# Kernel optimization log

Measured on AMD Instinct MI355X. Metric: run time of the kernel, lower is better.

Reference implementation:

```python
import jax, jax.numpy as jnp
import numpy as np
import math

NUM_HEADS = 16
NUM_KV_HEADS = 4
HEAD_DIM = 128
ROPE_THETA = 10000.0


def _rope(x, cos, sin):
    # x: [b, h, s, d]; cos/sin: [1, 1, s, d//2]
    half = x.shape[-1] // 2
    x1, x2 = x[..., :half], x[..., half:]
    return jnp.concatenate([x1 * cos - x2 * sin, x2 * cos + x1 * sin], axis=-1)


def setup_inputs() -> dict:
    key = jax.random.key(0)
    ks = jax.random.split(key, 5)
    B, S, H = 2, 2048, 2048
    scale_qk = (2.0 / (H + H)) ** 0.5
    scale_kv = (2.0 / (H + NUM_KV_HEADS * HEAD_DIM)) ** 0.5
    return {
        "hidden_states": jax.random.normal(ks[0], (B, S, H), jnp.float32),
        "Wq": jax.random.normal(ks[1], (NUM_HEADS * HEAD_DIM, H), jnp.float32) * scale_qk,
        "Wk": jax.random.normal(ks[2], (NUM_KV_HEADS * HEAD_DIM, H), jnp.float32) * scale_kv,
        "Wv": jax.random.normal(ks[3], (NUM_KV_HEADS * HEAD_DIM, H), jnp.float32) * scale_kv,
        "Wo": jax.random.normal(ks[4], (NUM_HEADS * HEAD_DIM, H), jnp.float32) * scale_qk,
    }


def reference(hidden_states, Wq, Wk, Wv, Wo):
    B, S, H = hidden_states.shape
    hd = HEAD_DIM

    q = (hidden_states @ Wq.T).reshape(B, S, NUM_HEADS, hd).transpose(0, 2, 1, 3)
    k = (hidden_states @ Wk.T).reshape(B, S, NUM_KV_HEADS, hd).transpose(0, 2, 1, 3)
    v = (hidden_states @ Wv.T).reshape(B, S, NUM_KV_HEADS, hd).transpose(0, 2, 1, 3)

    # RoPE (half-split variant, as in module)
    inv_freq = 1.0 / (ROPE_THETA ** (jnp.arange(0, hd, 2, dtype=jnp.float32) / hd))
    pos = jnp.arange(S, dtype=jnp.float32)
    freqs = pos[:, None] * inv_freq[None, :]           # [S, hd//2]
    cos = jnp.cos(freqs)[None, None]                   # [1,1,S,hd//2]
    sin = jnp.sin(freqs)[None, None]
    q = _rope(q, cos, sin)
    k = _rope(k, cos, sin)

    # GQA: repeat kv heads (repeat_interleave semantics)
    n_rep = NUM_HEADS // NUM_KV_HEADS
    k = jnp.repeat(k, n_rep, axis=1)
    v = jnp.repeat(v, n_rep, axis=1)

    scores = jnp.einsum("bhqd,bhkd->bhqk", q, k) / math.sqrt(hd)
    attn = jax.nn.softmax(scores, axis=-1)
    out = jnp.einsum("bhqk,bhkd->bhqd", attn, v)
    out = out.transpose(0, 2, 1, 3).reshape(B, S, NUM_HEADS * hd)
    return out @ Wo.T
```

## Files before the change

kernel.cpp:

```cpp
#include <hip/hip_runtime.h>
#include <cstdint>
#include <cstddef>

typedef __bf16 bf16x8 __attribute__((ext_vector_type(8)));
typedef __bf16 bf16x4 __attribute__((ext_vector_type(4)));
typedef float  f32x4  __attribute__((ext_vector_type(4)));

__device__ __forceinline__ void gload_lds16(const void* g, void* l) {
    __builtin_amdgcn_global_load_lds(
        (const __attribute__((address_space(1))) void*)g,
        (__attribute__((address_space(3))) void*)l, 16, 0, 0);
}

#define VM6B asm volatile("s_waitcnt vmcnt(6) lgkmcnt(0)\ns_barrier" ::: "memory")
#define VM4B asm volatile("s_waitcnt vmcnt(4) lgkmcnt(0)\ns_barrier" ::: "memory")
#define VM0B asm volatile("s_waitcnt vmcnt(0) lgkmcnt(0)\ns_barrier" ::: "memory")
#define BARO asm volatile("s_barrier" ::: "memory")
#define WAITB4 asm volatile("s_waitcnt vmcnt(4) lgkmcnt(0)\ns_barrier" ::: "memory")
#define WAITB0 asm volatile("s_waitcnt vmcnt(0) lgkmcnt(0)\ns_barrier" ::: "memory")

#define SEQ 2048
#define NH 16
#define NKV 4
#define HD 128

__global__ __launch_bounds__(256) void cvt_all(const float* __restrict__ hs,
                                               const float* __restrict__ wq,
                                               const float* __restrict__ wk,
                                               const float* __restrict__ wv,
                                               const float* __restrict__ wo,
                                               __bf16* __restrict__ hB,
                                               __bf16* __restrict__ WqkB,
                                               __bf16* __restrict__ WvB,
                                               __bf16* __restrict__ WoB) {
    int bid = blockIdx.x;
    const float* in; __bf16* out; int base;
    if (bid < 8192)        { in = hs; out = hB;                   base = bid; }
    else if (bid < 12288)  { in = wq; out = WqkB;                 base = bid - 8192; }
    else if (bid < 13312)  { in = wk; out = WqkB + 2048 * 2048;   base = bid - 12288; }
    else if (bid < 14336)  { in = wv; out = WvB;                  base = bid - 13312; }
    else                   { in = wo; out = WoB;                  base = bid - 14336; }
    int i = base * 256 + threadIdx.x;
    float4 v = ((const float4*)in)[i];
    bf16x4 o = { (__bf16)v.x, (__bf16)v.y, (__bf16)v.z, (__bf16)v.w };
    ((bf16x4*)out)[i] = o;
}

__device__ __forceinline__ void stage_half(const __bf16* __restrict__ M,
                                           char* dbuf, int bmn, int k0, int half,
                                           int wave, int lane) {
    char* hb = dbuf + (half & 1) * 32768 + (half >> 1) * 16384;
    int kbase = k0 + (half >> 1) * 32;
#pragma unroll
    for (int g = 0; g < 2; ++g) {
        int c = wave * 2 + g;
        int row = (c & 3) * 64 + lane;
        int ks = c >> 2;
        gload_lds16(M + (size_t)(bmn + row) * 2048 + kbase + ks * 8, hb + c * 1024);
    }
}

template <int KS, int MH>
__device__ __forceinline__ void phase_mfma(const __bf16* bA, const __bf16* bB,
                                           int quad, int l16, int wr128, int colbase,
                                           bf16x8 (&bq)[4], f32x4 acc[8][4]) {
    bf16x8 af[4];
#pragma unroll
    for (int ii = 0; ii < 4; ++ii)
        af[ii] = *(const bf16x8*)(bA + (KS * 4 + quad) * 2048 +
                                  (wr128 + (MH * 4 + ii) * 16 + l16) * 8);
    if (MH == 0) {
#pragma unroll
        for (int j = 0; j < 4; ++j)
            bq[j] = *(const bf16x8*)(bB + (KS * 4 + quad) * 2048 +
                                     (colbase + (j & 1) * 16 + (j >> 1) * 64 + l16) * 8);
    }
    __builtin_amdgcn_s_setprio(1);
#pragma unroll
    for (int ii = 0; ii < 4; ++ii)
#pragma unroll
        for (int j = 0; j < 4; ++j)
            acc[MH * 4 + ii][j] = __builtin_amdgcn_mfma_f32_16x16x32_bf16(
                af[ii], bq[j], acc[MH * 4 + ii][j], 0, 0, 0);
    __builtin_amdgcn_s_setprio(0);
}

__device__ __forceinline__ void gemm_core(const __bf16* __restrict__ A,
                                          const __bf16* __restrict__ B,
                                          char* lds, int bm, int bn,
                                          int wave, int lane, int quad, int l16,
                                          int wr128, int colbase, f32x4 acc[8][4]) {
    const int NT = 32;
    stage_half(A, lds, bm, 0, 0, wave, lane);
    stage_half(B, lds, bn, 0, 1, wave, lane);
    stage_half(A, lds, bm, 0, 2, wave, lane);
    stage_half(B, lds, bn, 0, 3, wave, lane);
    int cur = 0;
    for (int t = 0; t < NT - 1; ++t) {
        const __bf16* bA = (const __bf16*)(lds + cur * 65536);
        const __bf16* bB = (const __bf16*)(lds + cur * 65536 + 32768);
        char* nb = lds + (cur ^ 1) * 65536;
        int k1 = (t + 1) * 64;
        bf16x8 bq[4];
        stage_half(A, nb, bm, k1, 0, wave, lane);
        VM6B;
        phase_mfma<0, 0>(bA, bB, quad, l16, wr128, colbase, bq, acc);
        stage_half(B, nb, bn, k1, 1, wave, lane);
        BARO;
        phase_mfma<0, 1>(bA, bB, quad, l16, wr128, colbase, bq, acc);
        stage_half(A, nb, bm, k1, 2, wave, lane);
        VM6B;
        phase_mfma<1, 0>(bA, bB, quad, l16, wr128, colbase, bq, acc);
        stage_half(B, nb, bn, k1, 3, wave, lane);
        BARO;
        phase_mfma<1, 1>(bA, bB, quad, l16, wr128, colbase, bq, acc);
        cur ^= 1;
    }
    {
        const __bf16* bA = (const __bf16*)(lds + cur * 65536);
        const __bf16* bB = (const __bf16*)(lds + cur * 65536 + 32768);
        bf16x8 bq[4];
        VM4B;
        phase_mfma<0, 0>(bA, bB, quad, l16, wr128, colbase, bq, acc);
        phase_mfma<0, 1>(bA, bB, quad, l16, wr128, colbase, bq, acc);
        VM0B;
        phase_mfma<1, 0>(bA, bB, quad, l16, wr128, colbase, bq, acc);
        phase_mfma<1, 1>(bA, bB, quad, l16, wr128, colbase, bq, acc);
    }
}

__global__ __launch_bounds__(512, 2) void qkv_gemm(const __bf16* __restrict__ hB,
                                                   const __bf16* __restrict__ Wqk,
                                                   const __bf16* __restrict__ Wv,
                                                   __bf16* __restrict__ Qr,
                                                   __bf16* __restrict__ Kr,
                                                   __bf16* __restrict__ VT) {
    __shared__ __align__(16) char lds[2 * 65536];
    const int tid = threadIdx.x;
    const int wave = tid >> 6, lane = tid & 63;
    const int quad = lane >> 4, l16 = lane & 15;
    const int wr = wave >> 2, wc = wave & 3;
    int wg = blockIdx.y * 16 + blockIdx.x;
    wg = (wg & 7) * 24 + (wg >> 3);
    const int x = wg & 15, y = wg >> 4;
    const bool isVT = (y >= 10);
    const bool isQ = (y < 8);

    const __bf16* Amat = isVT ? Wv : hB;
    const __bf16* Bmat = isVT ? hB : (isQ ? Wqk : Wqk + 2048 * 2048);
    const int bm = isVT ? (y - 10) * 256 : x * 256;
    const int bn = isVT ? x * 256 : (isQ ? y * 256 : (y - 8) * 256);

    const int wr128 = wr * 128;
    const int colbase = (wc >> 1) * 128 + (wc & 1) * 32;

    f32x4 acc[8][4] = {};
    gemm_core(Amat, Bmat, lds, bm, bn, wave, lane, quad, l16, wr128, colbase, acc);

    if (isVT) {
#pragma unroll
        for (int i = 0; i < 8; ++i)
#pragma unroll
            for (int j = 0; j < 4; ++j) {
                int row = bm + wr128 + i * 16 + quad * 4;
                int col = bn + colbase + (j & 1) * 16 + (j >> 1) * 64 + l16;
#pragma unroll
                for (int r = 0; r < 4; ++r)
                    VT[(size_t)(row + r) * 4096 + col] = (__bf16)acc[i][j][r];
            }
    } else {
        __bf16* outp = isQ ? Qr : Kr;
        const float sc = isQ ? 0.1275255128608411f : 1.0f;
        const int nh = isQ ? NH : NKV;
        const int hh = (isQ ? y * 2 : (y - 8) * 2) + (wc >> 1);
#pragma unroll
        for (int j2 = 0; j2 < 2; ++j2) {
            int d = (wc & 1) * 32 + j2 * 16 + l16;
            float inv = exp2f(-(float)d * 0.2076205059304601f);
#pragma unroll
            for (int i = 0; i < 8; ++i)
#pragma unroll
                for (int r = 0; r < 4; ++r) {
                    int m = bm + wr128 + i * 16 + quad * 4 + r;
                    int s = m & (SEQ - 1), b = m >> 11;
                    float f = (float)s * inv;
                    float c = __cosf(f) * sc, sn = __sinf(f) * sc;
                    float x1 = acc[i][j2][r], x2 = acc[i][j2 + 2][r];
                    size_t rb = ((size_t)(b * nh + hh) * SEQ + s) * HD;
                    outp[rb + d]      = (__bf16)(x1 * c - x2 * sn);
                    outp[rb + d + 64] = (__bf16)(x2 * c + x1 * sn);
                }
        }
    }
}

__global__ __launch_bounds__(512, 1) void gemm_bt_f32(const __bf16* __restrict__ A,
                                                      const __bf16* __restrict__ W,
                                                      float* __restrict__ C) {
    __shared__ __align__(16) char lds[3 * 49152];
    const int tid = threadIdx.x;
    const int wave = tid >> 6, lane = tid & 63;
    const int quad = lane >> 4, l16 = lane & 15;
    const int wr = wave >> 2, wc = wave & 3;
    int wg = blockIdx.y * 32 + blockIdx.x;
    wg = (wg & 7) * 32 + (wg >> 3);
    const int bm = (wg & 31) * 128, bn = (wg >> 5) * 256;

    f32x4 acc[4][4] = {};

    auto stageT = [&](int sb, int k0) {
        char* dst = lds + sb * 49152;
#pragma unroll
        for (int tt = 0; tt < 6; ++tt) {
            int c = wave * 6 + tt;
            if (c < 16) {
                int row = ((c & 1) << 6) + lane;
                gload_lds16(A + (size_t)(bm + row) * 2048 + k0 + (c >> 1) * 8,
                            dst + c * 1024);
            } else {
                int vc = c - 16;
                int row = ((vc & 3) << 6) + lane;
                gload_lds16(W + (size_t)(bn + row) * 2048 + k0 + (vc >> 2) * 8,
                            dst + 16384 + vc * 1024);
            }
        }
    };

    auto computeT = [&](int cb2) {
        const __bf16* bA = (const __bf16*)(lds + cb2 * 49152);
        const __bf16* bB = bA + 8192;
#pragma unroll
        for (int ks = 0; ks < 2; ++ks) {
            bf16x8 af[4], bq[4];
#pragma unroll
            for (int i = 0; i < 4; ++i)
                af[i] = *(const bf16x8*)(bA + (ks * 4 + quad) * 1024 +
                                         (wr * 64 + i * 16 + l16) * 8);
#pragma unroll
            for (int j = 0; j < 4; ++j)
                bq[j] = *(const bf16x8*)(bB + (ks * 4 + quad) * 2048 +
                                         (wc * 64 + j * 16 + l16) * 8);
            __builtin_amdgcn_s_setprio(1);
#pragma unroll
            for (int i = 0; i < 4; ++i)
#pragma unroll
                for (int j = 0; j < 4; ++j)
                    acc[i][j] = __builtin_amdgcn_mfma_f32_16x16x32_bf16(
                        af[i], bq[j], acc[i][j], 0, 0, 0);
            __builtin_amdgcn_s_setprio(0);
        }
    };

    stageT(0, 0);
    stageT(1, 64);
    int cb = 0;
    for (int t = 0; t < 31; ++t) {
        VM6B;
        if (t < 30) {
            int sb = cb + 2; if (sb >= 3) sb -= 3;
            stageT(sb, (t + 2) * 64);
        }
        computeT(cb);
        if (++cb == 3) cb = 0;
    }
    VM0B;
    computeT(cb);

#pragma unroll
    for (int i = 0; i < 4; ++i)
#pragma unroll
        for (int j = 0; j < 4; ++j) {
            int row = bm + wr * 64 + i * 16 + quad * 4;
            int col = bn + wc * 64 + j * 16 + l16;
#pragma unroll
            for (int r = 0; r < 4; ++r)
                C[(size_t)(row + r) * 2048 + col] = acc[i][j][r];
        }
}

__global__ __launch_bounds__(256, 2) void attn_kernel(const __bf16* __restrict__ Q,
                                                      const __bf16* __restrict__ Kr,
                                                      const __bf16* __restrict__ VT,
                                                      __bf16* __restrict__ AO) {
    __shared__ __align__(16) char ring[3 * 16384];
    __shared__ __align__(16) __bf16 Pb[4][32][40];

    const int tid = threadIdx.x;
    const int wave = tid >> 6, lane = tid & 63;
    const int quad = lane >> 4, l16 = lane & 15;
    int wg = (blockIdx.z * 16 + blockIdx.y) * 16 + blockIdx.x;
    wg = (wg & 7) * 64 + (wg >> 3);
    const int x = wg & 15, h = (wg >> 4) & 15, b = wg >> 8;
    const int kv = h >> 2;
    const int qbase = x * 128 + wave * 32;

    bf16x8 qf[2][4];
#pragma unroll
    for (int qs = 0; qs < 2; ++qs) {
        const __bf16* Qp =
            Q + ((size_t)(b * NH + h) * SEQ + qbase + qs * 16 + l16) * HD + quad * 8;
#pragma unroll
        for (int kq = 0; kq < 4; ++kq) qf[qs][kq] = *(const bf16x8*)(Qp + kq * 32);
    }

    const __bf16* Kp = Kr + (size_t)(b * NKV + kv) * SEQ * HD;
    const __bf16* Vp = VT + (size_t)(kv * HD) * (2 * SEQ) + b * SEQ;

    f32x4 oacc[2][8] = {};
    float lpart[2] = {0.f, 0.f};

    auto stage = [&](int sb, int k0) {
        char* dst = ring + sb * 16384;
#pragma unroll
        for (int tt = 0; tt < 4; ++tt) {
            int c = wave * 4 + tt;
            if (c < 8) {
                gload_lds16(Kp + (size_t)(k0 + (lane & 31)) * HD +
                                (2 * c + (lane >> 5)) * 8,
                            dst + c * 1024);
            } else {
                int vc = c - 8;
                gload_lds16(Vp + (size_t)(((vc & 1) << 6) + lane) * (2 * SEQ) + k0 +
                                (vc >> 1) * 8,
                            dst + 8192 + vc * 1024);
            }
        }
    };

    auto compute = [&](int cb) {
        const __bf16* kt = (const __bf16*)(ring + cb * 16384);
        const __bf16* vt = kt + 4096;
#pragma unroll
        for (int mt = 0; mt < 2; ++mt) {
            f32x4 s0 = {0.f, 0.f, 0.f, 0.f}, s1 = {0.f, 0.f, 0.f, 0.f};
#pragma unroll
            for (int kq = 0; kq < 4; ++kq) {
                bf16x8 ka = *(const bf16x8*)(kt + (kq * 4 + quad) * 256 +
                                             (mt * 16 + l16) * 8);
                s0 = __builtin_amdgcn_mfma_f32_16x16x32_bf16(ka, qf[0][kq], s0, 0, 0, 0);
                s1 = __builtin_amdgcn_mfma_f32_16x16x32_bf16(ka, qf[1][kq], s1, 0, 0, 0);
            }
            bf16x4 pk0, pk1;
#pragma unroll
            for (int r = 0; r < 4; ++r) {
                float p0 = __builtin_amdgcn_exp2f(s0[r]);
                float p1 = __builtin_amdgcn_exp2f(s1[r]);
                lpart[0] += p0; lpart[1] += p1;
                pk0[r] = (__bf16)p0; pk1[r] = (__bf16)p1;
            }
            *(bf16x4*)&Pb[wave][l16][mt * 16 + quad * 4] = pk0;
            *(bf16x4*)&Pb[wave][16 + l16][mt * 16 + quad * 4] = pk1;
        }
        bf16x8 pb0 = *(const bf16x8*)&Pb[wave][l16][quad * 8];
        bf16x8 pb1 = *(const bf16x8*)&Pb[wave][16 + l16][quad * 8];
#pragma unroll
        for (int mt = 0; mt < 8; ++mt) {
            bf16x8 va = *(const bf16x8*)(vt + quad * 1024 + (mt * 16 + l16) * 8);
            oacc[0][mt] = __builtin_amdgcn_mfma_f32_16x16x32_bf16(
                va, pb0, oacc[0][mt], 0, 0, 0);
            oacc[1][mt] = __builtin_amdgcn_mfma_f32_16x16x32_bf16(
                va, pb1, oacc[1][mt], 0, 0, 0);
        }
    };

    stage(0, 0);
    stage(1, 32);
    int cb = 0;
    for (int t = 0; t < 63; ++t) {
        WAITB4;
        if (t < 62) {
            int sb = cb + 2; if (sb >= 3) sb -= 3;
            stage(sb, (t + 2) * 32);
        }
        compute(cb);
        if (++cb == 3) cb = 0;
    }
    WAITB0;
    compute(cb);

#pragma unroll
    for (int qs = 0; qs < 2; ++qs) {
        lpart[qs] += __shfl_xor(lpart[qs], 16);
        lpart[qs] += __shfl_xor(lpart[qs], 32);
        float inv = 1.f / lpart[qs];
        int q = qbase + qs * 16 + l16;
#pragma unroll
        for (int mt = 0; mt < 8; ++mt) {
            bf16x4 ov;
#pragma unroll
            for (int r = 0; r < 4; ++r) ov[r] = (__bf16)(oacc[qs][mt][r] * inv);
            *(bf16x4*)(AO + ((size_t)(b * SEQ + q)) * (NH * HD) + h * HD +
                       mt * 16 + quad * 4) = ov;
        }
    }
}

extern "C" void kernel_launch(void* const* d_in, const int* in_sizes, int n_in,
                              void* d_out, int out_size, void* d_ws, size_t ws_size,
                              hipStream_t stream) {
    const float* hs = (const float*)d_in[0];
    const float* Wq = (const float*)d_in[1];
    const float* Wk = (const float*)d_in[2];
    const float* Wv = (const float*)d_in[3];
    const float* Wo = (const float*)d_in[4];
    float* out = (float*)d_out;
    char* ws = (char*)d_ws;

    __bf16* Qr   = (__bf16*)(ws + 0);
    __bf16* Kr   = (__bf16*)(ws + 16777216);
    __bf16* VT   = (__bf16*)(ws + 20971520);
    __bf16* WoB  = (__bf16*)(ws + 25165824);
    __bf16* hB   = (__bf16*)(ws + 33554432);
    __bf16* WqkB = (__bf16*)(ws + 50331648);
    __bf16* WvB  = (__bf16*)(ws + 60817408);
    __bf16* AO   = (__bf16*)(ws + 33554432);

    cvt_all<<<18432, 256, 0, stream>>>(hs, Wq, Wk, Wv, Wo, hB, WqkB, WvB, WoB);

    qkv_gemm<<<dim3(16, 12), 512, 0, stream>>>(hB, WqkB, WvB, Qr, Kr, VT);

    attn_kernel<<<dim3(16, 16, 2), 256, 0, stream>>>(Qr, Kr, VT, AO);

    gemm_bt_f32<<<dim3(32, 8), 512, 0, stream>>>(AO, WoB, out);
}
```

Baseline: 332.9 us.

## Switch attention kernel MFMA from 16x16x32 to 32x32x16 tiles

Rewrites the attention inner loop to use 32x32x16 bf16 MFMA instructions instead of pairs of 16x16x32 ones, covering 32 queries per wave with a single accumulator tile. Q fragments, K/V LDS read patterns, the P staging layout, the row-sum reduction and the output store are all remapped to the 32x32 lane layout. The aim is fewer MFMA issues and fewer LDS fragment reads per key block. The cost is a different LDS access pattern that may cause bank conflicts, plus longer per-instruction latency in the dependent QK chain.

```diff
diff --git a/kernel.cpp b/kernel.cpp
--- a/kernel.cpp
+++ b/kernel.cpp
@@ -5,6 +5,7 @@
 typedef __bf16 bf16x8 __attribute__((ext_vector_type(8)));
 typedef __bf16 bf16x4 __attribute__((ext_vector_type(4)));
 typedef float  f32x4  __attribute__((ext_vector_type(4)));
+typedef float  f32x16 __attribute__((ext_vector_type(16)));
 
 __device__ __forceinline__ void gload_lds16(const void* g, void* l) {
     __builtin_amdgcn_global_load_lds(
@@ -287,27 +288,25 @@
 
     const int tid = threadIdx.x;
     const int wave = tid >> 6, lane = tid & 63;
-    const int quad = lane >> 4, l16 = lane & 15;
+    const int lo = lane & 31, hi = lane >> 5;
     int wg = (blockIdx.z * 16 + blockIdx.y) * 16 + blockIdx.x;
     wg = (wg & 7) * 64 + (wg >> 3);
     const int x = wg & 15, h = (wg >> 4) & 15, b = wg >> 8;
     const int kv = h >> 2;
     const int qbase = x * 128 + wave * 32;
 
-    bf16x8 qf[2][4];
-#pragma unroll
-    for (int qs = 0; qs < 2; ++qs) {
-        const __bf16* Qp =
-            Q + ((size_t)(b * NH + h) * SEQ + qbase + qs * 16 + l16) * HD + quad * 8;
-#pragma unroll
-        for (int kq = 0; kq < 4; ++kq) qf[qs][kq] = *(const bf16x8*)(Qp + kq * 32);
+    bf16x8 qf[8];
+    {
+        const __bf16* Qp = Q + ((size_t)(b * NH + h) * SEQ + qbase + lo) * HD;
+#pragma unroll
+        for (int t = 0; t < 8; ++t) qf[t] = *(const bf16x8*)(Qp + t * 16 + hi * 8);
     }
 
     const __bf16* Kp = Kr + (size_t)(b * NKV + kv) * SEQ * HD;
     const __bf16* Vp = VT + (size_t)(kv * HD) * (2 * SEQ) + b * SEQ;
 
-    f32x4 oacc[2][8] = {};
-    float lpart[2] = {0.f, 0.f};
+    f32x16 oacc[4] = {};
+    float lpart = 0.f;
 
     auto stage = [&](int sb, int k0) {
         char* dst = ring + sb * 16384;
@@ -330,36 +329,33 @@
     auto compute = [&](int cb) {
         const __bf16* kt = (const __bf16*)(ring + cb * 16384);
         const __bf16* vt = kt + 4096;
-#pragma unroll
-        for (int mt = 0; mt < 2; ++mt) {
-            f32x4 s0 = {0.f, 0.f, 0.f, 0.f}, s1 = {0.f, 0.f, 0.f, 0.f};
-#pragma unroll
-            for (int kq = 0; kq < 4; ++kq) {
-                bf16x8 ka = *(const bf16x8*)(kt + (kq * 4 + quad) * 256 +
-                                             (mt * 16 + l16) * 8);
-                s0 = __builtin_amdgcn_mfma_f32_16x16x32_bf16(ka, qf[0][kq], s0, 0, 0, 0);
-                s1 = __builtin_amdgcn_mfma_f32_16x16x32_bf16(ka, qf[1][kq], s1, 0, 0, 0);
-            }
-            bf16x4 pk0, pk1;
+        f32x16 s = {};
+#pragma unroll
+        for (int t = 0; t < 8; ++t) {
+            bf16x8 ka = *(const bf16x8*)(kt + ((2 * t + hi) * 32 + lo) * 8);
+            s = __builtin_amdgcn_mfma_f32_32x32x16_bf16(ka, qf[t], s, 0, 0, 0);
+        }
+#pragma unroll
+        for (int g = 0; g < 4; ++g) {
+            bf16x4 pk;
 #pragma unroll
             for (int r = 0; r < 4; ++r) {
-                float p0 = __builtin_amdgcn_exp2f(s0[r]);
-                float p1 = __builtin_amdgcn_exp2f(s1[r]);
-                lpart[0] += p0; lpart[1] += p1;
-                pk0[r] = (__bf16)p0; pk1[r] = (__bf16)p1;
-            }
-            *(bf16x4*)&Pb[wave][l16][mt * 16 + quad * 4] = pk0;
-            *(bf16x4*)&Pb[wave][16 + l16][mt * 16 + quad * 4] = pk1;
-        }
-        bf16x8 pb0 = *(const bf16x8*)&Pb[wave][l16][quad * 8];
-        bf16x8 pb1 = *(const bf16x8*)&Pb[wave][16 + l16][quad * 8];
-#pragma unroll
-        for (int mt = 0; mt < 8; ++mt) {
-            bf16x8 va = *(const bf16x8*)(vt + quad * 1024 + (mt * 16 + l16) * 8);
-            oacc[0][mt] = __builtin_amdgcn_mfma_f32_16x16x32_bf16(
-                va, pb0, oacc[0][mt], 0, 0, 0);
-            oacc[1][mt] = __builtin_amdgcn_mfma_f32_16x16x32_bf16(
-                va, pb1, oacc[1][mt], 0, 0, 0);
+                float p = __builtin_amdgcn_exp2f(s[g * 4 + r]);
+                lpart += p;
+                pk[r] = (__bf16)p;
+            }
+            *(bf16x4*)&Pb[wave][lo][g * 8 + hi * 4] = pk;
+        }
+#pragma unroll
+        for (int st = 0; st < 2; ++st) {
+            bf16x8 pbf = *(const bf16x8*)&Pb[wave][lo][st * 16 + hi * 8];
+#pragma unroll
+            for (int df = 0; df < 4; ++df) {
+                bf16x8 va = *(const bf16x8*)(vt + ((2 * st + hi) * 128 +
+                                                   df * 32 + lo) * 8);
+                oacc[df] = __builtin_amdgcn_mfma_f32_32x32x16_bf16(
+                    va, pbf, oacc[df], 0, 0, 0);
+            }
         }
     };
 
@@ -378,20 +374,21 @@
     WAITB0;
     compute(cb);
 
-#pragma unroll
-    for (int qs = 0; qs < 2; ++qs) {
-        lpart[qs] += __shfl_xor(lpart[qs], 16);
-        lpart[qs] += __shfl_xor(lpart[qs], 32);
-        float inv = 1.f / lpart[qs];
-        int q = qbase + qs * 16 + l16;
-#pragma unroll
-        for (int mt = 0; mt < 8; ++mt) {
-            bf16x4 ov;
-#pragma unroll
-            for (int r = 0; r < 4; ++r) ov[r] = (__bf16)(oacc[qs][mt][r] * inv);
-            *(bf16x4*)(AO + ((size_t)(b * SEQ + q)) * (NH * HD) + h * HD +
-                       mt * 16 + quad * 4) = ov;
-        }
+    lpart += __shfl_xor(lpart, 32);
+    float inv = 1.f / lpart;
+    {
+        int q = qbase + lo;
+        __bf16* aop = AO + ((size_t)(b * SEQ + q)) * (NH * HD) + h * HD;
+#pragma unroll
+        for (int df = 0; df < 4; ++df)
+#pragma unroll
+            for (int g = 0; g < 4; ++g) {
+                bf16x4 ov;
+#pragma unroll
+                for (int r = 0; r < 4; ++r)
+                    ov[r] = (__bf16)(oacc[df][g * 4 + r] * inv);
+                *(bf16x4*)(aop + df * 32 + g * 8 + hi * 4) = ov;
+            }
     }
 }
 
```

Measured after the change: 338.1 us. About the same (+1.6%).
